# Performance work log

Measured on AMD Instinct MI355X. Metric: run time of the kernel, lower is better.

## Reference

```python
import jax, jax.numpy as jnp
import numpy as np

D_MODEL = 2048
N_HEADS = 16
HEAD_DIM = D_MODEL // N_HEADS  # 128
HIDDEN = int(8 * D_MODEL / 3)  # 5461
EPS = 1e-6


def setup_inputs() -> dict:
    key = jax.random.key(0)
    ks = jax.random.split(key, 12)
    B, S = 2, 2048
    std = D_MODEL ** -0.5
    return {
        "x": jax.random.normal(ks[0], (B, S, D_MODEL), jnp.float32),
        "freq_cis": jax.random.normal(ks[1], (S, HEAD_DIM // 2, 2, 2), jnp.float32),
        "wq": jax.random.normal(ks[2], (D_MODEL, D_MODEL), jnp.float32) * std,
        "wk": jax.random.normal(ks[3], (D_MODEL, D_MODEL), jnp.float32) * std,
        "wv": jax.random.normal(ks[4], (D_MODEL, D_MODEL), jnp.float32) * std,
        "wo": jax.random.normal(ks[5], (D_MODEL, D_MODEL), jnp.float32) * std,
        "bo": jnp.zeros((D_MODEL,), jnp.float32),
        "w1": jax.random.normal(ks[6], (HIDDEN, D_MODEL), jnp.float32) * std,
        "w3": jax.random.normal(ks[7], (HIDDEN, D_MODEL), jnp.float32) * std,
        "w2": jax.random.normal(ks[8], (D_MODEL, HIDDEN), jnp.float32) * (HIDDEN ** -0.5),
        "g_attn": jnp.ones((D_MODEL,), jnp.float32),
        "g_ffn": jnp.ones((D_MODEL,), jnp.float32),
    }


def rmsnorm(x, g):
    xf = x.astype(jnp.float32)
    return xf * jax.lax.rsqrt(jnp.mean(xf * xf, axis=-1, keepdims=True) + EPS) * g


def rope(xq, xk, f):
    # xq/xk: [b, s, h, hd]; f: [s, hd/2, 2, 2]
    b, s, h, hd = xq.shape
    xq_ = xq.reshape(b, s, h, hd // 2, 2)
    xk_ = xk.reshape(b, s, h, hd // 2, 2)
    # out[b,s,h,i,j] = sum_k x[b,s,h,i,k] * f[s,i,j,k]
    q = jnp.einsum("bshik,sijk->bshij", xq_, f).reshape(b, s, h, hd)
    k = jnp.einsum("bshik,sijk->bshij", xk_, f).reshape(b, s, h, hd)
    return q, k


def reference(x, freq_cis, wq, wk, wv, wo, bo, w1, w3, w2, g_attn, g_ffn):
    b, s, d = x.shape
    h, hd = N_HEADS, HEAD_DIM
    scale = hd ** -0.5

    # --- attention sublayer ---
    xn = rmsnorm(x, g_attn)
    q = jnp.einsum("bsd,ed->bse", xn, wq).reshape(b, s, h, hd)
    k = jnp.einsum("bsd,ed->bse", xn, wk).reshape(b, s, h, hd)
    v = jnp.einsum("bsd,ed->bse", xn, wv).reshape(b, s, h, hd)
    q, k = rope(q, k, freq_cis[:s])
    attn = jnp.einsum("bqhd,bkhd->bhqk", q, k) * scale
    attn = jax.nn.softmax(attn, axis=-1)
    o = jnp.einsum("bhqk,bkhd->bqhd", attn, v).reshape(b, s, d)
    o = jnp.einsum("bsd,ed->bse", o, wo) + bo
    hres = x + o

    # --- SwiGLU FFN sublayer ---
    hn = rmsnorm(hres, g_ffn)
    x1 = jnp.einsum("bsd,hd->bsh", hn, w1)
    x3 = jnp.einsum("bsd,hd->bsh", hn, w3)
    ffn = jnp.einsum("bsh,dh->bsd", jax.nn.silu(x1) * x3, w2)
    return hres + ffn
```

## Files before the change

### kernel.cpp

```cpp
#include <hip/hip_runtime.h>

#define D_MODEL 2048
#define NHEADS 16
#define HDIM 128
#define HIDDEN_ 5461
#define HP2 5632
#define BATCH 2
#define SEQ 2048
#define MTOK 4096

typedef unsigned short u16;
typedef __attribute__((ext_vector_type(8))) short bf16x8;
typedef __attribute__((ext_vector_type(4))) float f32x4;
typedef __attribute__((ext_vector_type(4))) short s16x4;

__device__ __forceinline__ u16 f2b(float f) {
  union { float f; unsigned u; } v; v.f = f;
  return (u16)((v.u + 0x7FFFu + ((v.u >> 16) & 1u)) >> 16);
}
__device__ __forceinline__ float b2f(u16 u) {
  union { unsigned u; float f; } v; v.u = ((unsigned)u) << 16;
  return v.f;
}
__device__ __forceinline__ void gload16(const void* g, void* l) {
  __builtin_amdgcn_global_load_lds(
      (const __attribute__((address_space(1))) unsigned int*)g,
      (__attribute__((address_space(3))) unsigned int*)l, 16, 0, 0);
}

#define SB0() __builtin_amdgcn_sched_barrier(0)
#define BARRIER() do { SB0(); __builtin_amdgcn_s_barrier(); SB0(); } while (0)
#define LGKM0() do { asm volatile("s_waitcnt lgkmcnt(0)" ::: "memory"); SB0(); } while (0)

__global__ __launch_bounds__(256) void k_conv8(const float* __restrict__ src,
                                               u16* __restrict__ dst, int n8) {
  int stride = gridDim.x * 256;
  for (int i = blockIdx.x * 256 + threadIdx.x; i < n8; i += stride) {
    const float4* s = (const float4*)src + (size_t)i * 2;
    float4 a = s[0], b = s[1];
    bf16x8 o;
    o[0] = f2b(a.x); o[1] = f2b(a.y); o[2] = f2b(a.z); o[3] = f2b(a.w);
    o[4] = f2b(b.x); o[5] = f2b(b.y); o[6] = f2b(b.z); o[7] = f2b(b.w);
    ((bf16x8*)dst)[i] = o;
  }
}

__global__ __launch_bounds__(256) void k_conv3(const float* __restrict__ s0,
                                               const float* __restrict__ s1,
                                               const float* __restrict__ s2,
                                               u16* __restrict__ dst) {
  const int n8 = D_MODEL * D_MODEL / 8;
  int total = 3 * n8;
  int stride = gridDim.x * 256;
  for (int i = blockIdx.x * 256 + threadIdx.x; i < total; i += stride) {
    int seg = i >> 19, j = i & (n8 - 1);
    const float* s = (seg == 0) ? s0 : (seg == 1 ? s1 : s2);
    const float4* sp = (const float4*)s + (size_t)j * 2;
    float4 a = sp[0], b = sp[1];
    bf16x8 o;
    o[0] = f2b(a.x); o[1] = f2b(a.y); o[2] = f2b(a.z); o[3] = f2b(a.w);
    o[4] = f2b(b.x); o[5] = f2b(b.y); o[6] = f2b(b.z); o[7] = f2b(b.w);
    ((bf16x8*)dst)[i] = o;
  }
}

__global__ __launch_bounds__(256) void k_convrows(const float* __restrict__ src,
                                                  u16* __restrict__ dst,
                                                  int n8src, int n8dst) {
  int stride = gridDim.x * 256;
  for (int i = blockIdx.x * 256 + threadIdx.x; i < n8dst; i += stride) {
    bf16x8 o;
    if (i < n8src) {
      const float4* sp = (const float4*)src + (size_t)i * 2;
      float4 a = sp[0], b = sp[1];
      o[0] = f2b(a.x); o[1] = f2b(a.y); o[2] = f2b(a.z); o[3] = f2b(a.w);
      o[4] = f2b(b.x); o[5] = f2b(b.y); o[6] = f2b(b.z); o[7] = f2b(b.w);
    } else {
      o = (bf16x8){0, 0, 0, 0, 0, 0, 0, 0};
    }
    ((bf16x8*)dst)[i] = o;
  }
}

__global__ __launch_bounds__(256) void k_convpad(const float* __restrict__ src,
                                                 u16* __restrict__ dst,
                                                 int srows, int scols, int drows, int dcols) {
  size_t n = (size_t)drows * dcols;
  size_t stride = (size_t)gridDim.x * 256;
  for (size_t i = blockIdx.x * 256 + threadIdx.x; i < n; i += stride) {
    int r = (int)(i / dcols), c = (int)(i % dcols);
    float v = (r < srows && c < scols) ? src[(size_t)r * scols + c] : 0.f;
    dst[i] = f2b(v);
  }
}

__global__ __launch_bounds__(256) void k_silumul(u16* __restrict__ X1,
                                                 const u16* __restrict__ X3, int n8) {
  int stride = gridDim.x * 256;
  for (int i = blockIdx.x * 256 + threadIdx.x; i < n8; i += stride) {
    bf16x8 a = ((const bf16x8*)X1)[i];
    bf16x8 b = ((const bf16x8*)X3)[i];
    bf16x8 o;
#pragma unroll
    for (int e = 0; e < 8; e++) {
      float v1 = b2f((u16)a[e]);
      float v3 = b2f((u16)b[e]);
      float sig = 1.f / (1.f + __expf(-v1));
      o[e] = f2b(v1 * sig * v3);
    }
    ((bf16x8*)X1)[i] = o;
  }
}

__global__ __launch_bounds__(256) void k_rmsnorm(const float* __restrict__ X,
                                                 const float* __restrict__ G,
                                                 u16* __restrict__ Out) {
  int row = blockIdx.x;
  int tid = threadIdx.x;
  const float4* x4 = (const float4*)(X + (size_t)row * D_MODEL);
  float4 a = x4[tid * 2], b = x4[tid * 2 + 1];
  float ss = a.x * a.x + a.y * a.y + a.z * a.z + a.w * a.w +
             b.x * b.x + b.y * b.y + b.z * b.z + b.w * b.w;
#pragma unroll
  for (int off = 1; off < 64; off <<= 1) ss += __shfl_xor(ss, off);
  __shared__ float part[4];
  if ((tid & 63) == 0) part[tid >> 6] = ss;
  __syncthreads();
  float rstd = rsqrtf((part[0] + part[1] + part[2] + part[3]) * (1.0f / D_MODEL) + 1e-6f);
  const float4* g4 = (const float4*)G;
  float4 ga = g4[tid * 2], gb = g4[tid * 2 + 1];
  bf16x8 o;
  o[0] = f2b(a.x * rstd * ga.x); o[1] = f2b(a.y * rstd * ga.y);
  o[2] = f2b(a.z * rstd * ga.z); o[3] = f2b(a.w * rstd * ga.w);
  o[4] = f2b(b.x * rstd * gb.x); o[5] = f2b(b.y * rstd * gb.y);
  o[6] = f2b(b.z * rstd * gb.z); o[7] = f2b(b.w * rstd * gb.w);
  *((bf16x8*)(Out + (size_t)row * D_MODEL) + tid) = o;
}

template <int WN, int EPI>
__global__ __launch_bounds__(512, 2) void k_gemm2(const u16* __restrict__ A,
                                                  const u16* __restrict__ Bw,
                                                  const u16* __restrict__ Bw2,
                                                  void* __restrict__ O0,
                                                  void* __restrict__ O1,
                                                  void* __restrict__ O2,
                                                  const float* __restrict__ bias,
                                                  const float* __restrict__ res,
                                                  const u16* __restrict__ aux,
                                                  int M, int N, int K) {
  constexpr int BN = WN * 64;
  constexpr int PB = BN * 64;
  __shared__ __align__(128) char lds[65536 + 4 * PB];
  const int tid = threadIdx.x;
  const int w = tid >> 6, lane = tid & 63;
  const int lo = lane & 15, hi = lane >> 4;
  const int wr = w >> 2, wc = w & 3;

  const int ntN = N / BN;
  const int nwg = gridDim.x * gridDim.y;
  const int flat = blockIdx.y * gridDim.x + blockIdx.x;
  const int swz = (flat & 7) * (nwg >> 3) + (flat >> 3);
  const int tm = swz / ntN, tn = swz % ntN;
  const int m0 = tm * 256, n0 = tn * BN;

  const u16* bbase;
  if (EPI == 5)
    bbase = (n0 < 5632) ? Bw + (size_t)n0 * K : Bw2 + (size_t)(n0 - 5632) * K;
  else
    bbase = Bw + (size_t)n0 * K;

  auto stA = [&](int nb, int kk, int k0) {
#pragma unroll
    for (int j = 0; j < 2; ++j) {
      int row = j * 128 + (tid >> 2);
      const u16* g = A + (size_t)(m0 + row) * K + k0 + kk * 32 + (tid & 3) * 8;
      gload16(g, lds + nb * 32768 + kk * 16384 + j * 8192 + tid * 16);
    }
  };
  auto stB = [&](int nb, int kk, int k0) {
#pragma unroll
    for (int j = 0; j < WN / 2; ++j) {
      int row = j * 128 + (tid >> 2);
      const u16* g = bbase + (size_t)row * K + k0 + kk * 32 + (tid & 3) * 8;
      gload16(g, lds + 65536 + nb * 2 * PB + kk * PB + j * 8192 + tid * 16);
    }
  };
  auto ldA = [&](int buf, int kk, int mf) {
    return *(const bf16x8*)(lds + buf * 32768 + kk * 16384 +
                            (wr * 128 + mf * 16 + lo) * 64 + hi * 16);
  };
  auto ldB = [&](int buf, int kk, int nf) {
    return *(const bf16x8*)(lds + 65536 + buf * 2 * PB + kk * PB +
                            (wc * (WN * 16) + nf * 16 + lo) * 64 + hi * 16);
  };
#define VMCNT_CONFIRM()                                             \
  do {                                                              \
    if constexpr (WN == 4)                                          \
      asm volatile("s_waitcnt vmcnt(4)" ::: "memory");              \
    else                                                            \
      asm volatile("s_waitcnt vmcnt(3)" ::: "memory");              \
    SB0();                                                          \
  } while (0)

  f32x4 acc[8][WN];
#pragma unroll
  for (int i = 0; i < 8; i++)
#pragma unroll
    for (int j = 0; j < WN; j++) acc[i][j] = (f32x4){0.f, 0.f, 0.f, 0.f};

  stA(0, 0, 0);
  stB(0, 0, 0);
  stA(0, 1, 0);
  stB(0, 1, 0);
  VMCNT_CONFIRM();
  BARRIER();

  const int KT = K / 64;
  for (int kt = 0; kt < KT; ++kt) {
    const int buf = kt & 1, nb = buf ^ 1;
    int kn = (kt + 1) * 64;
    if (kn >= K) kn = 0;
    bf16x8 aF[4], bF[WN];

#pragma unroll
    for (int i = 0; i < 4; i++) aF[i] = ldA(buf, 0, i);
#pragma unroll
    for (int j = 0; j < WN; j++) bF[j] = ldB(buf, 0, j);
    stA(nb, 0, kn);
    BARRIER();
    LGKM0();
    __builtin_amdgcn_s_setprio(1);
#pragma unroll
    for (int i = 0; i < 4; i++)
#pragma unroll
      for (int j = 0; j < WN; j++)
        acc[i][j] = __builtin_amdgcn_mfma_f32_16x16x32_bf16(aF[i], bF[j], acc[i][j], 0, 0, 0);
    __builtin_amdgcn_s_setprio(0);
    BARRIER();

#pragma unroll
    for (int i = 0; i < 4; i++) aF[i] = ldA(buf, 0, 4 + i);
    stB(nb, 0, kn);
    VMCNT_CONFIRM();
    BARRIER();
    LGKM0();
    __builtin_amdgcn_s_setprio(1);
#pragma unroll
    for (int i = 0; i < 4; i++)
#pragma unroll
      for (int j = 0; j < WN; j++)
        acc[4 + i][j] = __builtin_amdgcn_mfma_f32_16x16x32_bf16(aF[i], bF[j], acc[4 + i][j], 0, 0, 0);
    __builtin_amdgcn_s_setprio(0);
    BARRIER();

#pragma unroll
    for (int i = 0; i < 4; i++) aF[i] = ldA(buf, 1, i);
#pragma unroll
    for (int j = 0; j < WN; j++) bF[j] = ldB(buf, 1, j);
    stA(nb, 1, kn);
    BARRIER();
    LGKM0();
    __builtin_amdgcn_s_setprio(1);
#pragma unroll
    for (int i = 0; i < 4; i++)
#pragma unroll
      for (int j = 0; j < WN; j++)
        acc[i][j] = __builtin_amdgcn_mfma_f32_16x16x32_bf16(aF[i], bF[j], acc[i][j], 0, 0, 0);
    __builtin_amdgcn_s_setprio(0);
    BARRIER();

#pragma unroll
    for (int i = 0; i < 4; i++) aF[i] = ldA(buf, 1, 4 + i);
    stB(nb, 1, kn);
    VMCNT_CONFIRM();
    BARRIER();
    LGKM0();
    __builtin_amdgcn_s_setprio(1);
#pragma unroll
    for (int i = 0; i < 4; i++)
#pragma unroll
      for (int j = 0; j < WN; j++)
        acc[4 + i][j] = __builtin_amdgcn_mfma_f32_16x16x32_bf16(aF[i], bF[j], acc[4 + i][j], 0, 0, 0);
    __builtin_amdgcn_s_setprio(0);
    BARRIER();
  }

  u16* qkvout = nullptr;
  int c0 = 0;
  if (EPI == 1) {
    int seg = n0 >> 11;
    qkvout = (u16*)(seg == 0 ? O0 : (seg == 1 ? O1 : O2));
    c0 = n0 & 2047;
  }
  u16* w13out = nullptr;
  int w13c0 = 0;
  if (EPI == 5) {
    w13out = (u16*)(n0 < 5632 ? O0 : O1);
    w13c0 = (n0 < 5632) ? n0 : n0 - 5632;
  }
#pragma unroll
  for (int i = 0; i < 8; i++) {
#pragma unroll
    for (int j = 0; j < WN; j++) {
      int colL = wc * (WN * 16) + j * 16 + lo;
#pragma unroll
      for (int r = 0; r < 4; r++) {
        int row = m0 + wr * 128 + i * 16 + hi * 4 + r;
        float v = acc[i][j][r];
        if (EPI == 0) {
          ((u16*)O0)[(size_t)row * N + n0 + colL] = f2b(v);
        } else if (EPI == 1) {
          qkvout[(size_t)row * 2048 + c0 + colL] = f2b(v);
        } else if (EPI == 2) {
          size_t idx = (size_t)row * N + n0 + colL;
          ((float*)O0)[idx] = v + bias[n0 + colL] + res[idx];
        } else if (EPI == 3) {
          size_t idx = (size_t)row * N + n0 + colL;
          ((float*)O0)[idx] = v + res[idx];
        } else if (EPI == 4) {
          size_t idx = (size_t)row * N + n0 + colL;
          float v1 = b2f(aux[idx]);
          float sig = 1.f / (1.f + __expf(-v1));
          ((u16*)O0)[idx] = f2b(v1 * sig * v);
        } else {
          w13out[(size_t)row * 5632 + w13c0 + colL] = f2b(v);
        }
      }
    }
  }
#undef VMCNT_CONFIRM
}

__global__ __launch_bounds__(256) void k_rope(u16* __restrict__ Qb, u16* __restrict__ Kb,
                                              const float* __restrict__ F) {
  int n = MTOK * (D_MODEL / 2);
  int stride = gridDim.x * 256;
  for (int t = blockIdx.x * 256 + threadIdx.x; t < n; t += stride) {
    int i = t & 63;
    int rest = t >> 6;
    int hh = rest & 15;
    int tok = rest >> 4;
    int s = tok & (SEQ - 1);
    float4 f = ((const float4*)F)[s * 64 + i];
    size_t off = (size_t)tok * D_MODEL + hh * HDIM + i * 2;
    float x0 = b2f(Qb[off]), x1 = b2f(Qb[off + 1]);
    Qb[off] = f2b(x0 * f.x + x1 * f.y);
    Qb[off + 1] = f2b(x0 * f.z + x1 * f.w);
    x0 = b2f(Kb[off]); x1 = b2f(Kb[off + 1]);
    Kb[off] = f2b(x0 * f.x + x1 * f.y);
    Kb[off + 1] = f2b(x0 * f.z + x1 * f.w);
  }
}

__global__ __launch_bounds__(256) void k_vt(const u16* __restrict__ V, u16* __restrict__ VT) {
  __shared__ u16 t[64][72];
  const int stile = blockIdx.x;
  const int bh = blockIdx.y;
  const int dz = blockIdx.z;
  const int b = bh >> 4, h = bh & 15;
  const int tok0 = b * SEQ + stile * 64;
  const int d0 = dz * 64;
  const int tid = threadIdx.x;
#pragma unroll
  for (int p = 0; p < 2; p++) {
    int idx = p * 256 + tid;
    int row = idx >> 3, seg = idx & 7;
    bf16x8 v = *(const bf16x8*)(V + (size_t)(tok0 + row) * D_MODEL + h * HDIM + d0 + seg * 8);
    *(bf16x8*)(&t[row][seg * 8]) = v;
  }
  __syncthreads();
#pragma unroll
  for (int p = 0; p < 2; p++) {
    int idx = p * 256 + tid;
    int dr = idx >> 3, seg = idx & 7;
    bf16x8 o;
#pragma unroll
    for (int e = 0; e < 8; e++) o[e] = t[seg * 8 + e][dr];
    *(bf16x8*)(VT + ((size_t)bh * HDIM + d0 + dr) * SEQ + stile * 64 + seg * 8) = o;
  }
}

__global__ __launch_bounds__(256) void k_flash3(const u16* __restrict__ Q,
                                                const u16* __restrict__ Kb,
                                                const u16* __restrict__ VT,
                                                u16* __restrict__ O) {
  __shared__ u16 Kt[64 * 128];
  __shared__ u16 Vt[128 * 64];
  __shared__ u16 Pl[4][2][16 * 72];
  const int tid = threadIdx.x;
  const int w = tid >> 6, lane = tid & 63;
  const int lo = lane & 15, hi = lane >> 4;
  const int qt = blockIdx.x, bh = blockIdx.y;
  const int b = bh >> 4, h = bh & 15;
  const size_t qrow0 = (size_t)b * SEQ + qt * 128 + w * 32;
  const float SC = 0.08838834764831845f * 1.4426950408889634f;

  bf16x8 aQ[2][4];
#pragma unroll
  for (int qg = 0; qg < 2; qg++)
#pragma unroll
    for (int kb = 0; kb < 4; kb++)
      aQ[qg][kb] = *(const bf16x8*)(Q + (qrow0 + qg * 16 + lo) * D_MODEL + h * HDIM + kb * 32 + hi * 8);

  float m_s[2] = {-3.0e38f, -3.0e38f}, l_s[2] = {0.f, 0.f};
  f32x4 oacc[2][8];
#pragma unroll
  for (int qg = 0; qg < 2; qg++)
#pragma unroll
    for (int d = 0; d < 8; d++) oacc[qg][d] = (f32x4){0.f, 0.f, 0.f, 0.f};

  const int krowL = tid >> 4;
  const int kslot = (tid & 15) ^ (krowL & 7);
  const int vrowL = tid >> 3;
  const int vslot = (tid & 7) ^ (vrowL & 7);
  const u16* Kbase = Kb + (size_t)b * SEQ * D_MODEL + h * HDIM;
  const u16* Vbase = VT + (size_t)bh * HDIM * SEQ;
  unsigned* Plw = (unsigned*)&Pl[w][0][0];

  for (int kt = 0; kt < SEQ / 64; kt++) {
    __syncthreads();
#pragma unroll
    for (int t = 0; t < 4; t++) {
      int row = t * 16 + krowL;
      const u16* g = Kbase + (size_t)(kt * 64 + row) * D_MODEL + kslot * 8;
      gload16(g, (char*)Kt + t * 4096 + tid * 16);
    }
#pragma unroll
    for (int t = 0; t < 4; t++) {
      int row = t * 32 + vrowL;
      const u16* g = Vbase + (size_t)row * SEQ + kt * 64 + vslot * 8;
      gload16(g, (char*)Vt + t * 4096 + tid * 16);
    }
    __syncthreads();

    f32x4 sf[2][4];
#pragma unroll
    for (int cb = 0; cb < 4; cb++) {
      bf16x8 kA[4];
#pragma unroll
      for (int kb = 0; kb < 4; kb++) {
        int ps = (kb * 4 + hi) ^ (lo & 7);
        kA[kb] = *(const bf16x8*)(Kt + (cb * 16 + lo) * 128 + ps * 8);
      }
#pragma unroll
      for (int qg = 0; qg < 2; qg++) {
        f32x4 s = (f32x4){0.f, 0.f, 0.f, 0.f};
#pragma unroll
        for (int kb = 0; kb < 4; kb++)
          s = __builtin_amdgcn_mfma_f32_16x16x32_bf16(kA[kb], aQ[qg][kb], s, 0, 0, 0);
        sf[qg][cb] = s;
      }
    }

    float tsc[2];
    bool ok = true;
#pragma unroll
    for (int qg = 0; qg < 2; qg++) {
      float t0 = fmaxf(fmaxf(sf[qg][0][0], sf[qg][0][1]), fmaxf(sf[qg][0][2], sf[qg][0][3]));
      float t1 = fmaxf(fmaxf(sf[qg][1][0], sf[qg][1][1]), fmaxf(sf[qg][1][2], sf[qg][1][3]));
      float t2 = fmaxf(fmaxf(sf[qg][2][0], sf[qg][2][1]), fmaxf(sf[qg][2][2], sf[qg][2][3]));
      float t3 = fmaxf(fmaxf(sf[qg][3][0], sf[qg][3][1]), fmaxf(sf[qg][3][2], sf[qg][3][3]));
      float t = fmaxf(fmaxf(t0, t1), fmaxf(t2, t3));
      t = fmaxf(t, __shfl_xor(t, 16));
      t = fmaxf(t, __shfl_xor(t, 32));
      tsc[qg] = t * SC;
      ok = ok && (tsc[qg] - m_s[qg] <= 11.5f);
    }
    bool skip = __all(ok);
#pragma unroll
    for (int qg = 0; qg < 2; qg++) {
      float mm = m_s[qg];
      if (!skip) {
        mm = fmaxf(m_s[qg], tsc[qg]);
        float alpha = exp2f(m_s[qg] - mm);
        l_s[qg] *= alpha;
#pragma unroll
        for (int d = 0; d < 8; d++) oacc[qg][d] *= alpha;
        m_s[qg] = mm;
      }
      float rs = 0.f;
#pragma unroll
      for (int cb = 0; cb < 4; cb++) {
        float p0 = exp2f(sf[qg][cb][0] * SC - mm);
        float p1 = exp2f(sf[qg][cb][1] * SC - mm);
        float p2 = exp2f(sf[qg][cb][2] * SC - mm);
        float p3 = exp2f(sf[qg][cb][3] * SC - mm);
        rs += (p0 + p1) + (p2 + p3);
        unsigned pk0, pk1;
        asm("v_cvt_pk_bf16_f32 %0, %1, %2" : "=v"(pk0) : "v"(p0), "v"(p1));
        asm("v_cvt_pk_bf16_f32 %0, %1, %2" : "=v"(pk1) : "v"(p2), "v"(p3));
        Plw[qg * 576 + lo * 36 + cb * 8 + hi * 2 + 0] = pk0;
        Plw[qg * 576 + lo * 36 + cb * 8 + hi * 2 + 1] = pk1;
      }
      rs += __shfl_xor(rs, 16);
      rs += __shfl_xor(rs, 32);
      l_s[qg] += rs;
    }
    LGKM0();

    bf16x8 aP[2][2];
#pragma unroll
    for (int qg = 0; qg < 2; qg++)
#pragma unroll
      for (int ks = 0; ks < 2; ks++)
        aP[qg][ks] = *(const bf16x8*)(&Pl[w][qg][lo * 72 + ks * 32 + hi * 8]);
#pragma unroll
    for (int db = 0; db < 8; db++) {
      bf16x8 vA[2];
#pragma unroll
      for (int ks = 0; ks < 2; ks++) {
        int ps = (ks * 4 + hi) ^ (lo & 7);
        vA[ks] = *(const bf16x8*)(Vt + (db * 16 + lo) * 64 + ps * 8);
      }
#pragma unroll
      for (int qg = 0; qg < 2; qg++)
#pragma unroll
        for (int ks = 0; ks < 2; ks++)
          oacc[qg][db] = __builtin_amdgcn_mfma_f32_16x16x32_bf16(vA[ks], aP[qg][ks], oacc[qg][db], 0, 0, 0);
    }
  }

#pragma unroll
  for (int qg = 0; qg < 2; qg++) {
    float inv = 1.f / l_s[qg];
    size_t rowoff = (qrow0 + qg * 16 + lo) * D_MODEL + h * HDIM;
#pragma unroll
    for (int db = 0; db < 8; db++) {
      s16x4 o;
#pragma unroll
      for (int r = 0; r < 4; r++) o[r] = (short)f2b(oacc[qg][db][r] * inv);
      *(s16x4*)(O + rowoff + db * 16 + hi * 4) = o;
    }
  }
}

extern "C" void kernel_launch(void* const* d_in, const int* in_sizes, int n_in,
                              void* d_out, int out_size, void* d_ws, size_t ws_size,
                              hipStream_t stream) {
  (void)in_sizes; (void)n_in; (void)out_size; (void)ws_size;
  const float* x  = (const float*)d_in[0];
  const float* fc = (const float*)d_in[1];
  const float* wq = (const float*)d_in[2];
  const float* wk = (const float*)d_in[3];
  const float* wv = (const float*)d_in[4];
  const float* wo = (const float*)d_in[5];
  const float* bo = (const float*)d_in[6];
  const float* w1 = (const float*)d_in[7];
  const float* w3 = (const float*)d_in[8];
  const float* w2 = (const float*)d_in[9];
  const float* ga = (const float*)d_in[10];
  const float* gf = (const float*)d_in[11];
  float* out = (float*)d_out;

  char* p = (char*)d_ws;
  auto alloc = [&](size_t bytes) { char* r = p; p += (bytes + 255) & ~(size_t)255; return r; };
  u16* xn  = (u16*)alloc((size_t)MTOK * D_MODEL * 2);
  u16* qb  = (u16*)alloc((size_t)MTOK * D_MODEL * 2);
  u16* kb  = (u16*)alloc((size_t)MTOK * D_MODEL * 2);
  u16* vb  = (u16*)alloc((size_t)MTOK * D_MODEL * 2);
  u16* x1  = (u16*)alloc((size_t)MTOK * HP2 * 2);
  u16* x3  = (u16*)alloc((size_t)MTOK * HP2 * 2);
  u16* wsl = (u16*)alloc((size_t)3 * D_MODEL * D_MODEL * 2);
  u16* vbt = xn;
  u16* ob  = vb;
  u16* hn  = qb;
  u16* w3b = kb;

  k_rmsnorm<<<MTOK, 256, 0, stream>>>(x, ga, xn);
  k_conv3<<<1536, 256, 0, stream>>>(wq, wk, wv, wsl);
  k_gemm2<4, 1><<<dim3(6144 / 256, MTOK / 256), 512, 0, stream>>>(
      xn, wsl, nullptr, qb, kb, vb, nullptr, nullptr, nullptr, MTOK, 6144, D_MODEL);
  k_rope<<<1024, 256, 0, stream>>>(qb, kb, fc);
  k_vt<<<dim3(SEQ / 64, BATCH * NHEADS, 2), 256, 0, stream>>>(vb, vbt);
  dim3 gfl(SEQ / 128, BATCH * NHEADS);
  k_flash3<<<gfl, 256, 0, stream>>>(qb, kb, vbt, ob);
  k_conv8<<<1024, 256, 0, stream>>>(wo, wsl, D_MODEL * D_MODEL / 8);
  k_gemm2<2, 2><<<dim3(2048 / 128, MTOK / 256), 512, 0, stream>>>(
      ob, wsl, nullptr, out, nullptr, nullptr, bo, x, nullptr, MTOK, D_MODEL, D_MODEL);

  k_rmsnorm<<<MTOK, 256, 0, stream>>>(out, gf, hn);
  k_convrows<<<1024, 256, 0, stream>>>(w1, wsl, HIDDEN_ * D_MODEL / 8, HP2 * D_MODEL / 8);
  k_convrows<<<1024, 256, 0, stream>>>(w3, w3b, HIDDEN_ * D_MODEL / 8, HP2 * D_MODEL / 8);
  k_gemm2<4, 5><<<dim3(11264 / 256, MTOK / 256), 512, 0, stream>>>(
      hn, wsl, w3b, x1, x3, nullptr, nullptr, nullptr, nullptr, MTOK, 11264, D_MODEL);
  k_silumul<<<2048, 256, 0, stream>>>(x1, x3, MTOK * HP2 / 8);
  k_convpad<<<1024, 256, 0, stream>>>(w2, wsl, D_MODEL, HIDDEN_, D_MODEL, HP2);
  k_gemm2<2, 3><<<dim3(2048 / 128, MTOK / 256), 512, 0, stream>>>(
      x1, wsl, nullptr, out, nullptr, nullptr, nullptr, out, nullptr, MTOK, D_MODEL, HP2);
}
```

Measured before the change: 753.6 us.

## Prefetch next K/V tile into registers during flash attention compute

Replaces the direct global-to-LDS K/V loads in the flash attention loop with register prefetching. The loads for tile kt+1 are issued before computing on tile kt and written to shared memory after compute, between barriers. This aims to hide global memory latency behind MFMA work. In exchange it adds register pressure (eight extra bf16x8 per thread) and an extra barrier per iteration. It assumes the BARRIER and SB0 macros are defined in the unseen part of the file.

```diff
diff --git a/kernel.cpp b/kernel.cpp
--- a/kernel.cpp
+++ b/kernel.cpp
@@ -380,7 +380,7 @@
   }
 }
 
-__global__ __launch_bounds__(256) void k_flash3(const u16* __restrict__ Q,
+__global__ __launch_bounds__(256) void k_flash4(const u16* __restrict__ Q,
                                                 const u16* __restrict__ Kb,
                                                 const u16* __restrict__ VT,
                                                 u16* __restrict__ O) {
@@ -417,21 +417,38 @@
   const u16* Vbase = VT + (size_t)bh * HDIM * SEQ;
   unsigned* Plw = (unsigned*)&Pl[w][0][0];
 
-  for (int kt = 0; kt < SEQ / 64; kt++) {
-    __syncthreads();
+  bf16x8 kreg[4], vreg[4];
+  auto issue = [&](int kt) {
 #pragma unroll
     for (int t = 0; t < 4; t++) {
       int row = t * 16 + krowL;
-      const u16* g = Kbase + (size_t)(kt * 64 + row) * D_MODEL + kslot * 8;
-      gload16(g, (char*)Kt + t * 4096 + tid * 16);
+      kreg[t] = *(const bf16x8*)(Kbase + (size_t)(kt * 64 + row) * D_MODEL + kslot * 8);
     }
 #pragma unroll
     for (int t = 0; t < 4; t++) {
       int row = t * 32 + vrowL;
-      const u16* g = Vbase + (size_t)row * SEQ + kt * 64 + vslot * 8;
-      gload16(g, (char*)Vt + t * 4096 + tid * 16);
-    }
-    __syncthreads();
+      vreg[t] = *(const bf16x8*)(Vbase + (size_t)row * SEQ + kt * 64 + vslot * 8);
+    }
+  };
+  auto commit = [&]() {
+#pragma unroll
+    for (int t = 0; t < 4; t++)
+      *(bf16x8*)((char*)Kt + t * 4096 + tid * 16) = kreg[t];
+#pragma unroll
+    for (int t = 0; t < 4; t++)
+      *(bf16x8*)((char*)Vt + t * 4096 + tid * 16) = vreg[t];
+  };
+
+  issue(0);
+  commit();
+  BARRIER();
+
+  const int NT = SEQ / 64;
+  for (int kt = 0; kt < NT; kt++) {
+    if (kt + 1 < NT) {
+      issue(kt + 1);
+      SB0();
+    }
 
     f32x4 sf[2][4];
 #pragma unroll
@@ -517,6 +534,12 @@
 #pragma unroll
         for (int ks = 0; ks < 2; ks++)
           oacc[qg][db] = __builtin_amdgcn_mfma_f32_16x16x32_bf16(vA[ks], aP[qg][ks], oacc[qg][db], 0, 0, 0);
+    }
+
+    if (kt + 1 < NT) {
+      BARRIER();
+      commit();
+      BARRIER();
     }
   }
 
@@ -573,7 +596,7 @@
   k_rope<<<1024, 256, 0, stream>>>(qb, kb, fc);
   k_vt<<<dim3(SEQ / 64, BATCH * NHEADS, 2), 256, 0, stream>>>(vb, vbt);
   dim3 gfl(SEQ / 128, BATCH * NHEADS);
-  k_flash3<<<gfl, 256, 0, stream>>>(qb, kb, vbt, ob);
+  k_flash4<<<gfl, 256, 0, stream>>>(qb, kb, vbt, ob);
   k_conv8<<<1024, 256, 0, stream>>>(wo, wsl, D_MODEL * D_MODEL / 8);
   k_gemm2<2, 2><<<dim3(2048 / 128, MTOK / 256), 512, 0, stream>>>(
       ob, wsl, nullptr, out, nullptr, nullptr, bo, x, nullptr, MTOK, D_MODEL, D_MODEL);
```

Measured after the change: 739.2 us. About the same (-1.9%).
